# Performance work log

Hardware: AMD Instinct MI355X
Metric: run time of the kernel (lower is better)

Reference implementation:

```python
import jax, jax.numpy as jnp
import numpy as np

B, T, R, A = 4, 40, 2000, 36864
H = W = 64
C = 256
PP = 7
RED = 16.0
NCLS = 21
NPOS = 64   # rois_per_image*B//4
NNEG = 192  # rois_per_image*B*3//4
DH = 1024

def _iou(b1, b2):
    # boxes are (top,left,bottom,right)
    t = jnp.maximum(b1[..., 0], b2[..., 0])
    l = jnp.maximum(b1[..., 1], b2[..., 1])
    b = jnp.minimum(b1[..., 2], b2[..., 2])
    r = jnp.minimum(b1[..., 3], b2[..., 3])
    inter = jnp.clip(b - t, 0.0) * jnp.clip(r - l, 0.0)
    a1 = (b1[..., 2] - b1[..., 0]) * (b1[..., 3] - b1[..., 1])
    a2 = (b2[..., 2] - b2[..., 0]) * (b2[..., 3] - b2[..., 1])
    return inter / (a1 + a2 - inter)

def _smooth_l1(p, t):
    d = jnp.abs(p - t)
    return jnp.mean(jnp.where(d < 1.0, 0.5 * d * d, d - 0.5))

def _roi_pool(fm, rois):
    # fm [B,C,H,W], rois [N,5] = (img_id, top,left,bottom,right) in feature-map coords
    fmt = jnp.transpose(fm, (0, 2, 3, 1))  # [B,H,W,C]
    n = rois[:, 0].astype(jnp.int32)[:, None, None]
    t, l, b, r = rois[:, 1], rois[:, 2], rois[:, 3], rois[:, 4]
    g = (jnp.arange(PP, dtype=fm.dtype) + 0.5) / PP
    ys = jnp.clip(t[:, None] + g * (b - t)[:, None], 0.0, H - 1.0)
    xs = jnp.clip(l[:, None] + g * (r - l)[:, None], 0.0, W - 1.0)
    y0 = jnp.floor(ys).astype(jnp.int32)
    x0 = jnp.floor(xs).astype(jnp.int32)
    y1 = jnp.minimum(y0 + 1, H - 1)
    x1 = jnp.minimum(x0 + 1, W - 1)
    wy = (ys - y0)[:, :, None, None]
    wx = (xs - x0)[:, None, :, None]
    def gat(yi, xi):
        return fmt[n, yi[:, :, None], xi[:, None, :], :]  # [N,PP,PP,C]
    v = (gat(y0, x0) * (1 - wy) * (1 - wx) + gat(y0, x1) * (1 - wy) * wx
         + gat(y1, x0) * wy * (1 - wx) + gat(y1, x1) * wy * wx)
    return v.reshape(v.shape[0], -1)  # [N, PP*PP*C]

def _forward(nms_reg, nms_cls, feature_maps, bboxes, classes, anchors, rpn_reg, rpn_cls, W1, b1, Wr, br, Wc, bc):
    # ---------------- RPN trainer: anchor/target matching ----------------
    iou_a = _iou(bboxes[:, :, None, :], anchors[None, None, :, :])   # [B,T,A]
    max_iou = jnp.max(iou_a, axis=1)                                  # [B,A]
    tidx = jnp.argmax(iou_a, axis=1)
    max_tgt = jnp.take_along_axis(bboxes, jnp.broadcast_to(tidx[:, :, None], (B, A, 4)), axis=1)
    mask = (max_iou > 0.5).reshape(-1)
    pos = jnp.nonzero(mask, size=128)[0]        # first 128 positives, flat order (matches cls[mask][:128])
    neg = jnp.nonzero(~mask, size=256 - B)[0]   # torch quirk: 256 - len(mask_matched) = 256 - B
    clsf = rpn_cls.reshape(-1)
    logits = jnp.concatenate([clsf[pos], clsf[neg]])
    lbl = jnp.concatenate([jnp.ones(128, dtype=logits.dtype), jnp.zeros(256 - B, dtype=logits.dtype)])
    rpn_cls_loss = jnp.mean(jnp.maximum(logits, 0) - logits * lbl + jnp.log1p(jnp.exp(-jnp.abs(logits))))
    anc_f = jnp.broadcast_to(anchors[None], (B, A, 4)).reshape(-1, 4)
    rpn_reg_loss = _smooth_l1(rpn_reg.reshape(-1, 4)[pos], max_tgt.reshape(-1, 4)[pos] - anc_f[pos]) / 4.0

    # ------------- RCNN trainer: proposal matching + sampling -------------
    iou_r = _iou(nms_reg[:, None, :, :], bboxes[:, :, None, :])  # [B,T,R]
    iou_m = jnp.max(iou_r, axis=1)                               # [B,R]
    ridx = jnp.argmax(iou_r, axis=1)
    iou_f = iou_m.reshape(-1)
    posr = jnp.nonzero(iou_f > 0.5, size=NPOS)[0]                # first NPOS positives, flat order
    negscore = jnp.where(iou_f <= 0.5, iou_f, -jnp.inf)
    negr = jax.lax.top_k(negscore, NNEG)[1]                      # negatives sorted by IoU descending
    cls_g = jnp.take_along_axis(classes, ridx, axis=1).reshape(-1)
    cls_s = jnp.concatenate([cls_g[posr], jnp.zeros(NNEG, dtype=cls_g.dtype)])
    imid = jnp.repeat(jnp.arange(B, dtype=nms_reg.dtype), R)
    nmsf = nms_reg.reshape(-1, 4)
    sel = jnp.concatenate([posr, negr])
    rois = jnp.concatenate([imid[sel][:, None], nmsf[sel]], axis=1)  # [256,5]
    feat = _roi_pool(feature_maps, rois)
    hmid = jax.nn.relu(feat @ W1 + b1)
    rreg = hmid @ Wr + br
    rcls = hmid @ Wc + bc
    logp = jax.nn.log_softmax(rcls, axis=-1)
    rcnn_cls_loss = -jnp.mean(jnp.take_along_axis(logp, cls_s[:, None], axis=1))
    posb = nmsf[posr]
    rounded = jnp.concatenate([jnp.floor(posb[:, :2] * RED), jnp.ceil(posb[:, 2:] * RED)], axis=1) / RED
    mb = jnp.take_along_axis(bboxes, jnp.broadcast_to(ridx[:, :, None], (B, R, 4)), axis=1).reshape(-1, 4)[posr]
    tgt = mb - rounded
    pr = rreg[:NPOS]
    rcnn_reg_loss = sum(_smooth_l1(pr[:, c], tgt[:, c]) for c in range(4)) / 4.0
    offset = sum(jnp.mean(jnp.abs(pr[:, c] - tgt[:, c])) for c in range(4)) / 4.0
    acc = jnp.mean((jnp.argmax(rcls[:NPOS], axis=-1) == cls_s[:NPOS]).astype(jnp.float32))
    return rpn_cls_loss, rpn_reg_loss, rcnn_cls_loss, rcnn_reg_loss, acc, offset

def _boxes(k, shape):
    k1, k2 = jax.random.split(k)
    c = jax.random.uniform(k1, shape + (2,), minval=10.0, maxval=54.0)
    h = jax.random.uniform(k2, shape + (2,), minval=3.0, maxval=8.0)
    return jnp.concatenate([c - h, c + h], axis=-1)  # (top,left,bottom,right)

def setup_inputs():
    key = jax.random.key(0)
    ks = jax.random.split(key, 13)
    base = _boxes(ks[0], (T,))
    shift = jax.random.uniform(ks[1], (B, T, 2), minval=-0.2, maxval=0.2)
    bboxes = base[None] + jnp.concatenate([shift, shift], axis=-1)  # guarantees >=128 RPN positives
    classes = jax.random.randint(ks[2], (B, T), 1, NCLS)
    anchors = _boxes(ks[3], (A,)).at[:T].set(base)
    nms_reg = _boxes(ks[4], (B, R))
    shift2 = jax.random.uniform(ks[5], (B, T, 2), minval=-0.1, maxval=0.1)
    nms_reg = nms_reg.at[:, :T].set(bboxes + jnp.concatenate([shift2, shift2], axis=-1))  # >=64 RCNN positives
    nms_cls = jax.random.normal(ks[6], (B, R))
    feature_maps = jax.random.normal(ks[7], (B, C, H, W))
    rpn_reg = 0.1 * jax.random.normal(ks[8], (B, A, 4))
    rpn_cls = jax.random.normal(ks[9], (B, A))
    D = PP * PP * C
    W1 = jax.random.normal(ks[10], (D, DH)) * float(1.0 / np.sqrt(D))
    b1 = jnp.zeros((DH,))
    Wr = jax.random.normal(ks[11], (DH, 4)) * float(1.0 / np.sqrt(DH))
    br = jnp.zeros((4,))
    Wc = jax.random.normal(ks[12], (DH, NCLS)) * float(1.0 / np.sqrt(DH))
    bc = jnp.zeros((NCLS,))
    return dict(nms_reg=nms_reg, nms_cls=nms_cls, feature_maps=feature_maps, bboxes=bboxes,
                classes=classes, anchors=anchors, rpn_reg=rpn_reg, rpn_cls=rpn_cls,
                W1=W1, b1=b1, Wr=Wr, br=br, Wc=Wc, bc=bc)

def reference(nms_reg, nms_cls, feature_maps, bboxes, classes, anchors, rpn_reg, rpn_cls, W1, b1, Wr, br, Wc, bc):
    return _forward(nms_reg, nms_cls, feature_maps, bboxes, classes, anchors, rpn_reg, rpn_cls, W1, b1, Wr, br, Wc, bc)
```

## Files before the change

kernel.cpp:

```cpp
#include <hip/hip_runtime.h>

typedef unsigned short u16;
typedef unsigned long long u64;

constexpr int cB = 4, cT = 40, cR = 2000, cA = 36864;
constexpr int cH = 64, cW = 64, cC = 256, cPP = 7;
constexpr int cNCLS = 21, cNPOS = 64, cNNEG = 192, cDH = 1024;
constexpr int cD = cPP * cPP * cC;
constexpr int cBA = cB * cA;
constexpr int cBR = cB * cR;
constexpr int NW64 = cBA / 64;
constexpr int SPLITS = 8;
constexpr int KCH = cD / SPLITS;
constexpr int NCH = KCH / 32;
constexpr unsigned POSKEY = 0x007FFFFFu;

constexpr size_t O_TIDX  = 0;
constexpr size_t O_MASKW = (size_t)cBA * 4;
constexpr size_t O_FMT   = 0;
constexpr size_t O_CPART = 0;
constexpr size_t O_PERS  = 8388608;
constexpr size_t O_SEL   = O_PERS;
constexpr size_t O_CLS   = O_PERS + 1024;
constexpr size_t O_ROIS  = O_PERS + 2048;
constexpr size_t O_TGT   = O_PERS + 6144;
constexpr size_t O_FEAT  = O_PERS + 8192;
constexpr size_t O_RREG  = O_FEAT + (size_t)256 * cD * 2;
constexpr size_t O_RCLS  = O_RREG + 4096;
constexpr size_t O_KEYS  = O_RCLS + 24576;
constexpr size_t O_RIDXG = O_KEYS + 32000;

__device__ __forceinline__ float b2f(u16 u) {
  return __uint_as_float(((unsigned)u) << 16);
}
__device__ __forceinline__ u16 f2b(float f) {
  unsigned x = __float_as_uint(f);
  unsigned r = x + 0x7FFFu + ((x >> 16) & 1u);
  return (u16)(r >> 16);
}
__device__ __forceinline__ unsigned f2key(float f) {
  unsigned b = __float_as_uint(f);
  return b ^ ((b & 0x80000000u) ? 0xFFFFFFFFu : 0x80000000u);
}

typedef __attribute__((ext_vector_type(8))) short short8;
typedef __attribute__((ext_vector_type(4))) float f32x4;

__global__ void k_ious(const float* __restrict__ bboxes, const float* __restrict__ anchors,
                       const float* __restrict__ nms_reg,
                       int* __restrict__ tidx, u64* __restrict__ maskw,
                       unsigned* __restrict__ keys, int* __restrict__ ridxg) {
  __shared__ float sb[cB * cT * 4];
  if (blockIdx.x < 576) {
    int b = blockIdx.x / 144;
    if (threadIdx.x < cT * 4) sb[threadIdx.x] = bboxes[b * cT * 4 + threadIdx.x];
    __syncthreads();
    int i = blockIdx.x * 256 + threadIdx.x;
    int a = i - b * cA;
    float4 av = ((const float4*)anchors)[a];
    float at = av.x, al = av.y, ab = av.z, ar = av.w;
    float area_a = (ab - at) * (ar - al);
    float best = -1.0f; int bi = 0;
    for (int t = 0; t < cT; ++t) {
      float bt = sb[t * 4], bl = sb[t * 4 + 1], bbv = sb[t * 4 + 2], brv = sb[t * 4 + 3];
      float ih = fmaxf(fminf(bbv, ab) - fmaxf(bt, at), 0.0f);
      float iw = fmaxf(fminf(brv, ar) - fmaxf(bl, al), 0.0f);
      float inter = ih * iw;
      float a1 = (bbv - bt) * (brv - bl);
      float iou = inter / (a1 + area_a - inter);
      if (iou > best) { best = iou; bi = t; }
    }
    tidx[i] = bi;
    u64 bal = __ballot(best > 0.5f);
    if ((threadIdx.x & 63) == 0) maskw[i >> 6] = bal;
  } else {
    for (int j = threadIdx.x; j < cB * cT * 4; j += 256) sb[j] = bboxes[j];
    __syncthreads();
    int i = (blockIdx.x - 576) * 256 + threadIdx.x;
    if (i >= cBR) return;
    int b = i / cR;
    float4 nv = ((const float4*)nms_reg)[i];
    float nt = nv.x, nl = nv.y, nb = nv.z, nr = nv.w;
    float area_n = (nb - nt) * (nr - nl);
    float best = -1.0f; int bi = 0;
    for (int t = 0; t < cT; ++t) {
      const float* bx = &sb[(b * cT + t) * 4];
      float ih = fmaxf(fminf(bx[2], nb) - fmaxf(bx[0], nt), 0.0f);
      float iw = fmaxf(fminf(bx[3], nr) - fmaxf(bx[1], nl), 0.0f);
      float inter = ih * iw;
      float a1 = (bx[2] - bx[0]) * (bx[3] - bx[1]);
      float iou = inter / (a1 + area_n - inter);
      if (iou > best) { best = iou; bi = t; }
    }
    keys[i] = (best <= 0.5f) ? f2key(best) : POSKEY;
    ridxg[i] = bi;
  }
}

__global__ __launch_bounds__(1024) void k_select(
    const u64* __restrict__ maskw, const int* __restrict__ tidx,
    const float* __restrict__ rpn_cls, const float* __restrict__ rpn_reg,
    const float* __restrict__ bboxes, const float* __restrict__ anchors,
    const unsigned* __restrict__ keysg, const int* __restrict__ ridxg,
    const float* __restrict__ nms_reg, const int* __restrict__ classes,
    int* __restrict__ sel, int* __restrict__ cls_s,
    float* __restrict__ rois, float* __restrict__ tgt,
    float* __restrict__ out) {
  __shared__ __align__(16) char smem[50688];
  __shared__ float s_scalF[2];
  __shared__ int s_scalI[3];
  int tid = threadIdx.x, lane = tid & 63, w = tid >> 6;
  u64 lmask = (1ULL << lane) - 1ULL;

  if (blockIdx.x == 0) {
    u64* s_w   = (u64*)smem;
    int* s_pre = (int*)(smem + 18432);
    int* s_cw  = (int*)(smem + 19008);
    int* s_pos = (int*)(smem + 19584);
    int* s_neg = (int*)(smem + 20096);
    for (int k = tid; k < NW64; k += 1024) s_w[k] = maskw[k];
    if (tid < 128) s_pos[tid] = 0;
    if (tid < 252) s_neg[tid] = 0;
    if (tid == 0) { s_scalF[0] = 0.0f; s_scalF[1] = 0.0f; }
    __syncthreads();
    if (tid < 144) {
      int c = 0;
      #pragma unroll
      for (int k2 = 0; k2 < 16; ++k2) c += __popcll(s_w[tid * 16 + k2]);
      s_cw[tid] = c;
    }
    __syncthreads();
    if (tid == 0) {
      int run = 0;
      for (int ch = 0; ch < 144; ++ch) { s_pre[ch] = run; run += s_cw[ch]; }
    }
    __syncthreads();
    for (int ch = w; ch < 144; ch += 16) {
      int pbase = s_pre[ch];
      int nbase = ch * 1024 - pbase;
      if (pbase >= 128 && nbase >= 252) continue;
      int pc = 0;
      #pragma unroll
      for (int s2 = 0; s2 < 16; ++s2) {
        u64 word = s_w[ch * 16 + s2];
        bool m = (word >> lane) & 1ULL;
        int prefP = __popcll(word & lmask);
        int idx = ch * 1024 + s2 * 64 + lane;
        if (m) {
          int g = pbase + pc + prefP;
          if (g < 128) s_pos[g] = idx;
        } else {
          int g = nbase + (s2 * 64 + lane) - (pc + prefP);
          if (g < 252) s_neg[g] = idx;
        }
        pc += __popcll(word);
      }
    }
    __syncthreads();
    if (tid < 380) {
      int flat; float lbl;
      if (tid < 128) { flat = s_pos[tid]; lbl = 1.0f; }
      else           { flat = s_neg[tid - 128]; lbl = 0.0f; }
      float l = rpn_cls[flat];
      float term = fmaxf(l, 0.0f) - l * lbl + log1pf(expf(-fabsf(l)));
      atomicAdd(&s_scalF[0], term);
    }
    if (tid < 512) {
      int j = tid >> 2, c = tid & 3;
      int flat = s_pos[j];
      int b = flat / cA, a = flat - b * cA;
      int t = tidx[flat];
      float p = rpn_reg[flat * 4 + c];
      float tg = bboxes[(b * cT + t) * 4 + c] - anchors[a * 4 + c];
      float d = fabsf(p - tg);
      float sl = (d < 1.0f) ? 0.5f * d * d : d - 0.5f;
      atomicAdd(&s_scalF[1], sl);
    }
    __syncthreads();
    if (tid == 0) {
      out[0] = s_scalF[0] / 380.0f;
      out[1] = s_scalF[1] / 512.0f / 4.0f;
    }
  } else {
    unsigned* s_key = (unsigned*)smem;
    int* s_hist = (int*)(smem + 32000);
    int* s_pc   = (int*)(smem + 48384);
    int* s_wsum = (int*)(smem + 48896);
    int* s_wsuf = (int*)(smem + 48960);
    int* s_posr = (int*)(smem + 49024);
    int* s_negr = (int*)(smem + 49280);

    for (int i = tid; i < cBR; i += 1024) s_key[i] = keysg[i];
    if (tid < 64) s_posr[tid] = 0;
    __syncthreads();

    {
      int myv = 0; int mypre[8];
      #pragma unroll
      for (int p = 0; p < 8; ++p) {
        int i = p * 1024 + tid;
        bool v = (i < cBR) && (s_key[i] == POSKEY);
        u64 bal = __ballot(v);
        if (lane == 0) s_pc[p * 16 + w] = __popcll(bal);
        mypre[p] = __popcll(bal & lmask);
        myv |= v ? (1 << p) : 0;
      }
      __syncthreads();
      if (tid == 0) {
        int run = 0;
        for (int k = 0; k < 128; ++k) { int t = s_pc[k]; s_pc[k] = run; run += t; }
      }
      __syncthreads();
      #pragma unroll
      for (int p = 0; p < 8; ++p) {
        if (myv & (1 << p)) {
          int g = s_pc[p * 16 + w] + mypre[p];
          if (g < 64) s_posr[g] = p * 1024 + tid;
        }
      }
    }

    unsigned thr = 0; int G = 0;
    int need = cNNEG;
    #pragma unroll
    for (int lvl = 0; lvl < 3; ++lvl) {
      __syncthreads();
      #pragma unroll
      for (int k = 0; k < 4; ++k) s_hist[tid * 4 + k] = 0;
      __syncthreads();
      #pragma unroll
      for (int p = 0; p < 8; ++p) {
        int i = p * 1024 + tid;
        if (i < cBR) {
          unsigned key = s_key[i];
          int bkt = -1;
          if (lvl == 0) bkt = key >> 20;
          else if (lvl == 1) { if ((key >> 20) == (thr >> 20)) bkt = (key >> 8) & 0xFFF; }
          else { if ((key >> 8) == (thr >> 8)) bkt = (key & 0xFF) << 4; }
          if (bkt >= 0) atomicAdd(&s_hist[bkt], 1);
        }
      }
      __syncthreads();
      int local0 = s_hist[tid * 4 + 0], local1 = s_hist[tid * 4 + 1];
      int local2 = s_hist[tid * 4 + 2], local3 = s_hist[tid * 4 + 3];
      int lsum = local0 + local1 + local2 + local3;
      int x = lsum;
      #pragma unroll
      for (int off = 1; off < 64; off <<= 1) {
        int t = __shfl_down(x, off, 64);
        if (lane + off < 64) x += t;
      }
      if (lane == 0) s_wsum[w] = x;
      __syncthreads();
      if (tid == 0) {
        int run = 0;
        for (int wi = 15; wi >= 0; --wi) { s_wsuf[wi] = run; run += s_wsum[wi]; }
      }
      __syncthreads();
      int above = s_wsuf[w] + (x - lsum);
      int run = above;
      int loc[4] = {local3, local2, local1, local0};
      #pragma unroll
      for (int j = 0; j < 4; ++j) {
        int S = run + loc[j];
        if (run < need && S >= need) { s_scalI[0] = tid * 4 + (3 - j); s_scalI[1] = run; }
        run = S;
      }
      __syncthreads();
      int bS = s_scalI[0], ov = s_scalI[1];
      if (lvl == 0) thr = ((unsigned)bS) << 20;
      else if (lvl == 1) thr |= ((unsigned)bS) << 8;
      else thr |= ((unsigned)bS) >> 4;
      G += ov;
      need -= ov;
    }

    if (tid == 0) s_scalI[2] = 0;
    __syncthreads();
    #pragma unroll
    for (int p = 0; p < 8; ++p) {
      int i = p * 1024 + tid;
      if (i < cBR && s_key[i] > thr) {
        int slot = atomicAdd(&s_scalI[2], 1);
        s_negr[slot] = i;
      }
    }
    {
      __syncthreads();
      int myv = 0; int mypre[8];
      #pragma unroll
      for (int p = 0; p < 8; ++p) {
        int i = p * 1024 + tid;
        bool v = (i < cBR) && (s_key[i] == thr);
        u64 bal = __ballot(v);
        if (lane == 0) s_pc[p * 16 + w] = __popcll(bal);
        mypre[p] = __popcll(bal & lmask);
        myv |= v ? (1 << p) : 0;
      }
      __syncthreads();
      if (tid == 0) {
        int run = 0;
        for (int k = 0; k < 128; ++k) { int t = s_pc[k]; s_pc[k] = run; run += t; }
      }
      __syncthreads();
      #pragma unroll
      for (int p = 0; p < 8; ++p) {
        if (myv & (1 << p)) {
          int g = s_pc[p * 16 + w] + mypre[p];
          if (g < need) s_negr[G + g] = p * 1024 + tid;
        }
      }
    }
    __syncthreads();

    if (tid < 256) {
      int flat = (tid < 64) ? s_posr[tid] : s_negr[tid - 64];
      sel[tid] = flat;
      int b = flat / cR;
      #pragma unroll
      for (int c = 0; c < 4; ++c) rois[tid * 4 + c] = nms_reg[flat * 4 + c];
      cls_s[tid] = (tid < 64) ? classes[b * cT + ridxg[flat]] : 0;
      if (tid < 64) {
        int mt = ridxg[flat];
        #pragma unroll
        for (int c = 0; c < 4; ++c) {
          float v = nms_reg[flat * 4 + c];
          float rr = ((c < 2) ? floorf(v * 16.0f) : ceilf(v * 16.0f)) / 16.0f;
          float mbv = bboxes[(b * cT + mt) * 4 + c];
          tgt[tid * 4 + c] = mbv - rr;
        }
      }
    }
  }
}

__global__ __launch_bounds__(256) void k_fmt(const float* __restrict__ fm, u16* __restrict__ fmt) {
  __shared__ float tile[64][65];
  int b = blockIdx.z;
  int p0 = blockIdx.x * 64, c0 = blockIdx.y * 64;
  int t = threadIdx.x;
  int pL = (t & 15) * 4, cL = t >> 4;
  #pragma unroll
  for (int i = 0; i < 4; ++i) {
    int c = cL + i * 16;
    float4 v = *(const float4*)&fm[((size_t)b * cC + c0 + c) * (cH * cW) + p0 + pL];
    tile[c][pL] = v.x; tile[c][pL + 1] = v.y; tile[c][pL + 2] = v.z; tile[c][pL + 3] = v.w;
  }
  __syncthreads();
  int pW = t >> 2, cg = (t & 3) * 16;
  unsigned pk[8];
  #pragma unroll
  for (int j = 0; j < 8; ++j) {
    unsigned lo = f2b(tile[cg + 2 * j][pW]);
    unsigned hi = f2b(tile[cg + 2 * j + 1][pW]);
    pk[j] = lo | (hi << 16);
  }
  u16* dst = &fmt[((size_t)b * (cH * cW) + p0 + pW) * cC + c0 + cg];
  *(uint4*)dst = *(uint4*)&pk[0];
  *(uint4*)(dst + 8) = *(uint4*)&pk[4];
}

__global__ void k_roi_pool(const u16* __restrict__ fmt, const float* __restrict__ rois,
                           const int* __restrict__ sel, u16* __restrict__ feat) {
  int j = blockIdx.x;
  int py = blockIdx.y;
  int c = threadIdx.x;
  int flat = sel[j];
  int n = flat / cR;
  float t = rois[j * 4 + 0], l = rois[j * 4 + 1];
  float bb = rois[j * 4 + 2], r = rois[j * 4 + 3];
  const u16* base = fmt + (size_t)n * (cH * cW) * cC;
  float gy = (py + 0.5f) / (float)cPP;
  float ys = fminf(fmaxf(t + gy * (bb - t), 0.0f), 63.0f);
  int y0 = (int)floorf(ys);
  int y1 = min(y0 + 1, 63);
  float wy = ys - (float)y0;
  #pragma unroll
  for (int px = 0; px < cPP; ++px) {
    float gx = (px + 0.5f) / (float)cPP;
    float xs = fminf(fmaxf(l + gx * (r - l), 0.0f), 63.0f);
    int x0 = (int)floorf(xs);
    int x1 = min(x0 + 1, 63);
    float wx = xs - (float)x0;
    float f00 = b2f(base[(y0 * cW + x0) * cC + c]);
    float f01 = b2f(base[(y0 * cW + x1) * cC + c]);
    float f10 = b2f(base[(y1 * cW + x0) * cC + c]);
    float f11 = b2f(base[(y1 * cW + x1) * cC + c]);
    float v = f00 * (1.0f - wy) * (1.0f - wx) + f01 * (1.0f - wy) * wx +
              f10 * wy * (1.0f - wx) + f11 * wy * wx;
    feat[((size_t)j * 49 + py * cPP + px) * cC + c] = f2b(v);
  }
}

__global__ __launch_bounds__(256) void k_gemm1(const u16* __restrict__ feat, const float* __restrict__ W1,
                                               float* __restrict__ Cpart) {
  __shared__ u16 As[64][40];
  __shared__ u16 Bs[32][40];
  int tid = threadIdx.x;
  int n0 = blockIdx.x * 32;
  int kb0 = blockIdx.y * KCH;
  int m0 = blockIdx.z * 64;
  int lane = tid & 63, w = tid >> 6;
  int r = lane & 15, q = lane >> 4;
  f32x4 acc[2] = {};
  int arow = tid >> 2, ako = (tid & 3) * 8;
  int bn2 = tid & 31, bkq = tid >> 5;

  uint4 rA0, rA1;
  float rb0[4], rb1[4];
  auto loadAB = [&](int kc, uint4& ra, float* rb) {
    int kb = kb0 + kc * 32;
    ra = *(const uint4*)&feat[(size_t)(m0 + arow) * cD + kb + ako];
    const float* bp = &W1[(size_t)(kb + bkq * 4) * cDH + n0 + bn2];
    rb[0] = bp[0]; rb[1] = bp[cDH]; rb[2] = bp[2 * cDH]; rb[3] = bp[3 * cDH];
  };
  auto step = [&](int kc, uint4& ra, float* rb, bool pf) {
    __syncthreads();
    *(uint4*)&As[arow][ako] = ra;
    union { u16 u[4]; uint2 v; } pb;
    #pragma unroll
    for (int j = 0; j < 4; ++j) pb.u[j] = f2b(rb[j]);
    *(uint2*)&Bs[bn2][bkq * 4] = pb.v;
    if (pf) loadAB(kc + 2, ra, rb);
    __syncthreads();
    short8 a = *(const short8*)&As[w * 16 + r][q * 8];
    #pragma unroll
    for (int nt = 0; nt < 2; ++nt) {
      short8 bfr = *(const short8*)&Bs[nt * 16 + r][q * 8];
      acc[nt] = __builtin_amdgcn_mfma_f32_16x16x32_bf16(a, bfr, acc[nt], 0, 0, 0);
    }
  };

  loadAB(0, rA0, rb0);
  loadAB(1, rA1, rb1);
  for (int kc = 0; kc < NCH - 1; kc += 2) {
    step(kc, rA0, rb0, kc + 2 < NCH);
    step(kc + 1, rA1, rb1, kc + 3 < NCH);
  }
  step(NCH - 1, rA0, rb0, false);

  float* Cp = Cpart + (size_t)blockIdx.y * 256 * cDH;
  #pragma unroll
  for (int nt = 0; nt < 2; ++nt) {
    #pragma unroll
    for (int rg = 0; rg < 4; ++rg) {
      int row = m0 + w * 16 + q * 4 + rg;
      int col = n0 + nt * 16 + r;
      Cp[(size_t)row * cDH + col] = acc[nt][rg];
    }
  }
}

__global__ __launch_bounds__(256) void k_heads(
    const float* __restrict__ Cpart, const float* __restrict__ b1,
    const float* __restrict__ Wr, const float* __restrict__ br,
    const float* __restrict__ Wc, const float* __restrict__ bc,
    float* __restrict__ rreg, float* __restrict__ rcls) {
  __shared__ float sacc[25];
  int row = blockIdx.x, tid = threadIdx.x, lane = tid & 63;
  if (tid < 25) sacc[tid] = 0.0f;
  __syncthreads();
  int k0 = tid * 4;
  float4 h = *(const float4*)&b1[k0];
  #pragma unroll
  for (int s = 0; s < SPLITS; ++s) {
    float4 c = *(const float4*)&Cpart[(size_t)s * 256 * cDH + (size_t)row * cDH + k0];
    h.x += c.x; h.y += c.y; h.z += c.z; h.w += c.w;
  }
  float hv[4] = {fmaxf(h.x, 0.f), fmaxf(h.y, 0.f), fmaxf(h.z, 0.f), fmaxf(h.w, 0.f)};
  float part[25];
  #pragma unroll
  for (int c = 0; c < 25; ++c) part[c] = 0.0f;
  #pragma unroll
  for (int j = 0; j < 4; ++j) {
    float4 wr = *(const float4*)&Wr[(k0 + j) * 4];
    part[0] += hv[j] * wr.x; part[1] += hv[j] * wr.y;
    part[2] += hv[j] * wr.z; part[3] += hv[j] * wr.w;
    const float* wc = &Wc[(k0 + j) * 21];
    #pragma unroll
    for (int c = 0; c < 21; ++c) part[4 + c] += hv[j] * wc[c];
  }
  #pragma unroll
  for (int off = 32; off; off >>= 1) {
    #pragma unroll
    for (int c = 0; c < 25; ++c) part[c] += __shfl_down(part[c], off, 64);
  }
  if (lane == 0) {
    #pragma unroll
    for (int c = 0; c < 25; ++c) atomicAdd(&sacc[c], part[c]);
  }
  __syncthreads();
  if (tid < 4) rreg[row * 4 + tid] = sacc[tid] + br[tid];
  else if (tid < 25) rcls[row * 21 + (tid - 4)] = sacc[tid] + bc[tid - 4];
}

__global__ void k_final(const float* __restrict__ rcls, const float* __restrict__ rreg,
                        const int* __restrict__ cls_s, const float* __restrict__ tgt,
                        float* __restrict__ out) {
  __shared__ float s_cls, s_acc, s_sl1, s_off;
  int tid = threadIdx.x;
  if (tid == 0) { s_cls = 0.0f; s_acc = 0.0f; s_sl1 = 0.0f; s_off = 0.0f; }
  __syncthreads();
  {
    int row = tid;
    float m = -INFINITY;
    for (int c = 0; c < cNCLS; ++c) m = fmaxf(m, rcls[row * cNCLS + c]);
    float sum = 0.0f;
    for (int c = 0; c < cNCLS; ++c) sum += expf(rcls[row * cNCLS + c] - m);
    float lse = m + logf(sum);
    float closs = lse - rcls[row * cNCLS + cls_s[row]];
    atomicAdd(&s_cls, closs);
  }
  if (tid < 64) {
    int am = 0; float bv = rcls[tid * cNCLS];
    for (int c = 1; c < cNCLS; ++c) {
      float v = rcls[tid * cNCLS + c];
      if (v > bv) { bv = v; am = c; }
    }
    if (am == cls_s[tid]) atomicAdd(&s_acc, 1.0f);
    float sl = 0.0f, of = 0.0f;
    #pragma unroll
    for (int c = 0; c < 4; ++c) {
      float d = fabsf(rreg[tid * 4 + c] - tgt[tid * 4 + c]);
      sl += (d < 1.0f) ? 0.5f * d * d : d - 0.5f;
      of += d;
    }
    atomicAdd(&s_sl1, sl);
    atomicAdd(&s_off, of);
  }
  __syncthreads();
  if (tid == 0) {
    out[2] = s_cls / 256.0f;
    out[3] = s_sl1 / 256.0f;
    out[4] = s_acc / 64.0f;
    out[5] = s_off / 256.0f;
  }
}

extern "C" void kernel_launch(void* const* d_in, const int* in_sizes, int n_in,
                              void* d_out, int out_size, void* d_ws, size_t ws_size,
                              hipStream_t stream) {
  const float* nms_reg = (const float*)d_in[0];
  const float* fm      = (const float*)d_in[2];
  const float* bboxes  = (const float*)d_in[3];
  const int*   classes = (const int*)d_in[4];
  const float* anchors = (const float*)d_in[5];
  const float* rpn_reg = (const float*)d_in[6];
  const float* rpn_cls = (const float*)d_in[7];
  const float* W1      = (const float*)d_in[8];
  const float* b1      = (const float*)d_in[9];
  const float* Wr      = (const float*)d_in[10];
  const float* br      = (const float*)d_in[11];
  const float* Wc      = (const float*)d_in[12];
  const float* bc      = (const float*)d_in[13];
  float* out = (float*)d_out;
  char* ws = (char*)d_ws;

  int*      tidx  = (int*)(ws + O_TIDX);
  u64*      maskw = (u64*)(ws + O_MASKW);
  u16*      fmt   = (u16*)(ws + O_FMT);
  float*    Cpart = (float*)(ws + O_CPART);
  int*      sel   = (int*)(ws + O_SEL);
  int*      clss  = (int*)(ws + O_CLS);
  float*    rois  = (float*)(ws + O_ROIS);
  float*    tgt   = (float*)(ws + O_TGT);
  u16*      feat  = (u16*)(ws + O_FEAT);
  float*    rreg  = (float*)(ws + O_RREG);
  float*    rcls  = (float*)(ws + O_RCLS);
  unsigned* keys  = (unsigned*)(ws + O_KEYS);
  int*      ridxg = (int*)(ws + O_RIDXG);

  k_ious<<<576 + 32, 256, 0, stream>>>(bboxes, anchors, nms_reg, tidx, maskw, keys, ridxg);
  k_select<<<2, 1024, 0, stream>>>(maskw, tidx, rpn_cls, rpn_reg, bboxes, anchors,
                                   keys, ridxg, nms_reg, classes, sel, clss, rois, tgt, out);
  k_fmt<<<dim3(cH * cW / 64, cC / 64, cB), 256, 0, stream>>>(fm, fmt);
  k_roi_pool<<<dim3(256, cPP), 256, 0, stream>>>(fmt, rois, sel, feat);
  k_gemm1<<<dim3(32, SPLITS, 4), 256, 0, stream>>>(feat, W1, Cpart);
  k_heads<<<256, 256, 0, stream>>>(Cpart, b1, Wr, br, Wc, bc, rreg, rcls);
  k_final<<<1, 256, 0, stream>>>(rcls, rreg, clss, tgt, out);
}
```

Measured before the change: 201.3 us.

## Fuse fmt transpose into IoU kernel, fold final loss into heads, retile GEMM

Merges the feature-map transpose/bf16 conversion into the IoU kernel as extra blocks, and folds the loss reduction into the heads kernel, which now accumulates into the output with atomics. Output zeroing moves to k_select. Launch count drops as a result. The split-K GEMM now uses 128-wide K tiles with XOR-swizzled LDS, register prefetch and 14 splits, to cut synchronisation per MFMA and raise parallelism. The workspace is relaid so the transposed map no longer aliases earlier buffers. Float atomics make the loss sums order-dependent.

```diff
diff --git a/kernel.cpp b/kernel.cpp
--- a/kernel.cpp
+++ b/kernel.cpp
@@ -10,25 +10,23 @@
 constexpr int cBA = cB * cA;
 constexpr int cBR = cB * cR;
 constexpr int NW64 = cBA / 64;
-constexpr int SPLITS = 8;
+constexpr int SPLITS = 14;
 constexpr int KCH = cD / SPLITS;
-constexpr int NCH = KCH / 32;
+constexpr int BK = 128;
+constexpr int NITER = KCH / BK;
 constexpr unsigned POSKEY = 0x007FFFFFu;
 
 constexpr size_t O_TIDX  = 0;
-constexpr size_t O_MASKW = (size_t)cBA * 4;
-constexpr size_t O_FMT   = 0;
-constexpr size_t O_CPART = 0;
-constexpr size_t O_PERS  = 8388608;
-constexpr size_t O_SEL   = O_PERS;
-constexpr size_t O_CLS   = O_PERS + 1024;
-constexpr size_t O_ROIS  = O_PERS + 2048;
-constexpr size_t O_TGT   = O_PERS + 6144;
-constexpr size_t O_FEAT  = O_PERS + 8192;
-constexpr size_t O_RREG  = O_FEAT + (size_t)256 * cD * 2;
-constexpr size_t O_RCLS  = O_RREG + 4096;
-constexpr size_t O_KEYS  = O_RCLS + 24576;
-constexpr size_t O_RIDXG = O_KEYS + 32000;
+constexpr size_t O_MASKW = 589824;
+constexpr size_t O_KEYS  = 608256;
+constexpr size_t O_RIDXG = 640256;
+constexpr size_t O_SEL   = 672256;
+constexpr size_t O_CLS   = 673280;
+constexpr size_t O_ROIS  = 674304;
+constexpr size_t O_TGT   = 678400;
+constexpr size_t O_FMT   = 1048576;
+constexpr size_t O_FEAT  = O_FMT + 8388608;
+constexpr size_t O_CPART = O_FEAT + 6422528;
 
 __device__ __forceinline__ float b2f(u16 u) {
   return __uint_as_float(((unsigned)u) << 16);
@@ -46,16 +44,20 @@
 typedef __attribute__((ext_vector_type(8))) short short8;
 typedef __attribute__((ext_vector_type(4))) float f32x4;
 
-__global__ void k_ious(const float* __restrict__ bboxes, const float* __restrict__ anchors,
-                       const float* __restrict__ nms_reg,
-                       int* __restrict__ tidx, u64* __restrict__ maskw,
-                       unsigned* __restrict__ keys, int* __restrict__ ridxg) {
-  __shared__ float sb[cB * cT * 4];
-  if (blockIdx.x < 576) {
-    int b = blockIdx.x / 144;
+__global__ __launch_bounds__(256) void k_front(
+    const float* __restrict__ bboxes, const float* __restrict__ anchors,
+    const float* __restrict__ nms_reg, const float* __restrict__ fm,
+    int* __restrict__ tidx, u64* __restrict__ maskw,
+    unsigned* __restrict__ keys, int* __restrict__ ridxg,
+    u16* __restrict__ fmt) {
+  __shared__ float sfm[64 * 65];
+  int bid = blockIdx.x;
+  if (bid < 576) {
+    float* sb = sfm;
+    int b = bid / 144;
     if (threadIdx.x < cT * 4) sb[threadIdx.x] = bboxes[b * cT * 4 + threadIdx.x];
     __syncthreads();
-    int i = blockIdx.x * 256 + threadIdx.x;
+    int i = bid * 256 + threadIdx.x;
     int a = i - b * cA;
     float4 av = ((const float4*)anchors)[a];
     float at = av.x, al = av.y, ab = av.z, ar = av.w;
@@ -73,10 +75,11 @@
     tidx[i] = bi;
     u64 bal = __ballot(best > 0.5f);
     if ((threadIdx.x & 63) == 0) maskw[i >> 6] = bal;
-  } else {
+  } else if (bid < 608) {
+    float* sb = sfm;
     for (int j = threadIdx.x; j < cB * cT * 4; j += 256) sb[j] = bboxes[j];
     __syncthreads();
-    int i = (blockIdx.x - 576) * 256 + threadIdx.x;
+    int i = (bid - 576) * 256 + threadIdx.x;
     if (i >= cBR) return;
     int b = i / cR;
     float4 nv = ((const float4*)nms_reg)[i];
@@ -94,6 +97,32 @@
     }
     keys[i] = (best <= 0.5f) ? f2key(best) : POSKEY;
     ridxg[i] = bi;
+  } else {
+    int f = bid - 608;
+    int b = f >> 8;
+    int c0 = ((f >> 6) & 3) * 64;
+    int p0 = (f & 63) * 64;
+    int t = threadIdx.x;
+    int pL = (t & 15) * 4, cL = t >> 4;
+    #pragma unroll
+    for (int i = 0; i < 4; ++i) {
+      int c = cL + i * 16;
+      float4 v = *(const float4*)&fm[((size_t)b * cC + c0 + c) * (cH * cW) + p0 + pL];
+      sfm[c * 65 + pL] = v.x; sfm[c * 65 + pL + 1] = v.y;
+      sfm[c * 65 + pL + 2] = v.z; sfm[c * 65 + pL + 3] = v.w;
+    }
+    __syncthreads();
+    int pW = t >> 2, cg = (t & 3) * 16;
+    unsigned pk[8];
+    #pragma unroll
+    for (int j = 0; j < 8; ++j) {
+      unsigned lo = f2b(sfm[(cg + 2 * j) * 65 + pW]);
+      unsigned hi = f2b(sfm[(cg + 2 * j + 1) * 65 + pW]);
+      pk[j] = lo | (hi << 16);
+    }
+    u16* dst = &fmt[((size_t)b * (cH * cW) + p0 + pW) * cC + c0 + cg];
+    *(uint4*)dst = *(uint4*)&pk[0];
+    *(uint4*)(dst + 8) = *(uint4*)&pk[4];
   }
 }
 
@@ -113,6 +142,7 @@
   u64 lmask = (1ULL << lane) - 1ULL;
 
   if (blockIdx.x == 0) {
+    if (tid < 4) out[2 + tid] = 0.0f;
     u64* s_w   = (u64*)smem;
     int* s_pre = (int*)(smem + 18432);
     int* s_cw  = (int*)(smem + 19008);
@@ -332,32 +362,6 @@
       }
     }
   }
-}
-
-__global__ __launch_bounds__(256) void k_fmt(const float* __restrict__ fm, u16* __restrict__ fmt) {
-  __shared__ float tile[64][65];
-  int b = blockIdx.z;
-  int p0 = blockIdx.x * 64, c0 = blockIdx.y * 64;
-  int t = threadIdx.x;
-  int pL = (t & 15) * 4, cL = t >> 4;
-  #pragma unroll
-  for (int i = 0; i < 4; ++i) {
-    int c = cL + i * 16;
-    float4 v = *(const float4*)&fm[((size_t)b * cC + c0 + c) * (cH * cW) + p0 + pL];
-    tile[c][pL] = v.x; tile[c][pL + 1] = v.y; tile[c][pL + 2] = v.z; tile[c][pL + 3] = v.w;
-  }
-  __syncthreads();
-  int pW = t >> 2, cg = (t & 3) * 16;
-  unsigned pk[8];
-  #pragma unroll
-  for (int j = 0; j < 8; ++j) {
-    unsigned lo = f2b(tile[cg + 2 * j][pW]);
-    unsigned hi = f2b(tile[cg + 2 * j + 1][pW]);
-    pk[j] = lo | (hi << 16);
-  }
-  u16* dst = &fmt[((size_t)b * (cH * cW) + p0 + pW) * cC + c0 + cg];
-  *(uint4*)dst = *(uint4*)&pk[0];
-  *(uint4*)(dst + 8) = *(uint4*)&pk[4];
 }
 
 __global__ void k_roi_pool(const u16* __restrict__ fmt, const float* __restrict__ rois,
@@ -394,8 +398,8 @@
 
 __global__ __launch_bounds__(256) void k_gemm1(const u16* __restrict__ feat, const float* __restrict__ W1,
                                                float* __restrict__ Cpart) {
-  __shared__ u16 As[64][40];
-  __shared__ u16 Bs[32][40];
+  __shared__ u16 As[64 * 128];
+  __shared__ u16 Bs[32 * 128];
   int tid = threadIdx.x;
   int n0 = blockIdx.x * 32;
   int kb0 = blockIdx.y * KCH;
@@ -403,41 +407,53 @@
   int lane = tid & 63, w = tid >> 6;
   int r = lane & 15, q = lane >> 4;
   f32x4 acc[2] = {};
-  int arow = tid >> 2, ako = (tid & 3) * 8;
-  int bn2 = tid & 31, bkq = tid >> 5;
-
-  uint4 rA0, rA1;
-  float rb0[4], rb1[4];
-  auto loadAB = [&](int kc, uint4& ra, float* rb) {
-    int kb = kb0 + kc * 32;
-    ra = *(const uint4*)&feat[(size_t)(m0 + arow) * cD + kb + ako];
-    const float* bp = &W1[(size_t)(kb + bkq * 4) * cDH + n0 + bn2];
-    rb[0] = bp[0]; rb[1] = bp[cDH]; rb[2] = bp[2 * cDH]; rb[3] = bp[3 * cDH];
+
+  int am = tid >> 2;
+  int aj0 = (tid & 3) * 4;
+  int bn = tid & 31;
+  int bkg = tid >> 5;
+
+  uint4 ra[4];
+  float rb[16];
+  auto loadAB = [&](int it) {
+    int kb = kb0 + it * BK;
+    const u16* ap = &feat[(size_t)(m0 + am) * cD + kb];
+    #pragma unroll
+    for (int i = 0; i < 4; ++i) ra[i] = *(const uint4*)(ap + (aj0 + i) * 8);
+    const float* bp = &W1[(size_t)(kb + bkg * 16) * cDH + n0 + bn];
+    #pragma unroll
+    for (int j = 0; j < 16; ++j) rb[j] = bp[(size_t)j * cDH];
   };
-  auto step = [&](int kc, uint4& ra, float* rb, bool pf) {
-    __syncthreads();
-    *(uint4*)&As[arow][ako] = ra;
-    union { u16 u[4]; uint2 v; } pb;
-    #pragma unroll
-    for (int j = 0; j < 4; ++j) pb.u[j] = f2b(rb[j]);
-    *(uint2*)&Bs[bn2][bkq * 4] = pb.v;
-    if (pf) loadAB(kc + 2, ra, rb);
-    __syncthreads();
-    short8 a = *(const short8*)&As[w * 16 + r][q * 8];
-    #pragma unroll
-    for (int nt = 0; nt < 2; ++nt) {
-      short8 bfr = *(const short8*)&Bs[nt * 16 + r][q * 8];
-      acc[nt] = __builtin_amdgcn_mfma_f32_16x16x32_bf16(a, bfr, acc[nt], 0, 0, 0);
-    }
-  };
-
-  loadAB(0, rA0, rb0);
-  loadAB(1, rA1, rb1);
-  for (int kc = 0; kc < NCH - 1; kc += 2) {
-    step(kc, rA0, rb0, kc + 2 < NCH);
-    step(kc + 1, rA1, rb1, kc + 3 < NCH);
-  }
-  step(NCH - 1, rA0, rb0, false);
+
+  loadAB(0);
+  for (int it = 0; it < NITER; ++it) {
+    __syncthreads();
+    #pragma unroll
+    for (int i = 0; i < 4; ++i) {
+      int c = aj0 + i;
+      *(uint4*)&As[am * 128 + ((c ^ (am & 15)) << 3)] = ra[i];
+    }
+    #pragma unroll
+    for (int s = 0; s < 2; ++s) {
+      union { u16 u[8]; uint4 v; } pb;
+      #pragma unroll
+      for (int j = 0; j < 8; ++j) pb.u[j] = f2b(rb[s * 8 + j]);
+      int c = bkg * 2 + s;
+      *(uint4*)&Bs[bn * 128 + ((c ^ (bn & 15)) << 3)] = pb.v;
+    }
+    __syncthreads();
+    if (it + 1 < NITER) loadAB(it + 1);
+    #pragma unroll
+    for (int ks = 0; ks < 4; ++ks) {
+      int ca = ks * 4 + q;
+      short8 a = *(const short8*)&As[(w * 16 + r) * 128 + ((ca ^ r) << 3)];
+      #pragma unroll
+      for (int nt = 0; nt < 2; ++nt) {
+        short8 bfr = *(const short8*)&Bs[(nt * 16 + r) * 128 + ((ca ^ r) << 3)];
+        acc[nt] = __builtin_amdgcn_mfma_f32_16x16x32_bf16(a, bfr, acc[nt], 0, 0, 0);
+      }
+    }
+  }
 
   float* Cp = Cpart + (size_t)blockIdx.y * 256 * cDH;
   #pragma unroll
@@ -455,7 +471,8 @@
     const float* __restrict__ Cpart, const float* __restrict__ b1,
     const float* __restrict__ Wr, const float* __restrict__ br,
     const float* __restrict__ Wc, const float* __restrict__ bc,
-    float* __restrict__ rreg, float* __restrict__ rcls) {
+    const int* __restrict__ cls_s, const float* __restrict__ tgt,
+    float* __restrict__ out) {
   __shared__ float sacc[25];
   int row = blockIdx.x, tid = threadIdx.x, lane = tid & 63;
   if (tid < 25) sacc[tid] = 0.0f;
@@ -490,50 +507,34 @@
     for (int c = 0; c < 25; ++c) atomicAdd(&sacc[c], part[c]);
   }
   __syncthreads();
-  if (tid < 4) rreg[row * 4 + tid] = sacc[tid] + br[tid];
-  else if (tid < 25) rcls[row * 21 + (tid - 4)] = sacc[tid] + bc[tid - 4];
-}
-
-__global__ void k_final(const float* __restrict__ rcls, const float* __restrict__ rreg,
-                        const int* __restrict__ cls_s, const float* __restrict__ tgt,
-                        float* __restrict__ out) {
-  __shared__ float s_cls, s_acc, s_sl1, s_off;
-  int tid = threadIdx.x;
-  if (tid == 0) { s_cls = 0.0f; s_acc = 0.0f; s_sl1 = 0.0f; s_off = 0.0f; }
-  __syncthreads();
-  {
-    int row = tid;
+  if (tid == 0) {
+    int cls = cls_s[row];
     float m = -INFINITY;
-    for (int c = 0; c < cNCLS; ++c) m = fmaxf(m, rcls[row * cNCLS + c]);
+    float vals[21];
+    #pragma unroll
+    for (int c = 0; c < 21; ++c) { vals[c] = sacc[4 + c] + bc[c]; m = fmaxf(m, vals[c]); }
     float sum = 0.0f;
-    for (int c = 0; c < cNCLS; ++c) sum += expf(rcls[row * cNCLS + c] - m);
+    #pragma unroll
+    for (int c = 0; c < 21; ++c) sum += expf(vals[c] - m);
     float lse = m + logf(sum);
-    float closs = lse - rcls[row * cNCLS + cls_s[row]];
-    atomicAdd(&s_cls, closs);
-  }
-  if (tid < 64) {
-    int am = 0; float bv = rcls[tid * cNCLS];
-    for (int c = 1; c < cNCLS; ++c) {
-      float v = rcls[tid * cNCLS + c];
-      if (v > bv) { bv = v; am = c; }
-    }
-    if (am == cls_s[tid]) atomicAdd(&s_acc, 1.0f);
+    atomicAdd(&out[2], (lse - vals[cls]) * (1.0f / 256.0f));
+    if (row < 64) {
+      int am2 = 0; float bv = vals[0];
+      #pragma unroll
+      for (int c = 1; c < 21; ++c) if (vals[c] > bv) { bv = vals[c]; am2 = c; }
+      if (am2 == cls) atomicAdd(&out[4], 1.0f / 64.0f);
+    }
+  }
+  if (tid == 1 && row < 64) {
     float sl = 0.0f, of = 0.0f;
     #pragma unroll
     for (int c = 0; c < 4; ++c) {
-      float d = fabsf(rreg[tid * 4 + c] - tgt[tid * 4 + c]);
+      float d = fabsf((sacc[c] + br[c]) - tgt[row * 4 + c]);
       sl += (d < 1.0f) ? 0.5f * d * d : d - 0.5f;
       of += d;
     }
-    atomicAdd(&s_sl1, sl);
-    atomicAdd(&s_off, of);
-  }
-  __syncthreads();
-  if (tid == 0) {
-    out[2] = s_cls / 256.0f;
-    out[3] = s_sl1 / 256.0f;
-    out[4] = s_acc / 64.0f;
-    out[5] = s_off / 256.0f;
+    atomicAdd(&out[3], sl * (1.0f / 256.0f));
+    atomicAdd(&out[5], of * (1.0f / 256.0f));
   }
 }
 
@@ -558,24 +559,21 @@
 
   int*      tidx  = (int*)(ws + O_TIDX);
   u64*      maskw = (u64*)(ws + O_MASKW);
-  u16*      fmt   = (u16*)(ws + O_FMT);
-  float*    Cpart = (float*)(ws + O_CPART);
+  unsigned* keys  = (unsigned*)(ws + O_KEYS);
+  int*      ridxg = (int*)(ws + O_RIDXG);
   int*      sel   = (int*)(ws + O_SEL);
   int*      clss  = (int*)(ws + O_CLS);
   float*    rois  = (float*)(ws + O_ROIS);
   float*    tgt   = (float*)(ws + O_TGT);
+  u16*      fmt   = (u16*)(ws + O_FMT);
   u16*      feat  = (u16*)(ws + O_FEAT);
-  float*    rreg  = (float*)(ws + O_RREG);
-  float*    rcls  = (float*)(ws + O_RCLS);
-  unsigned* keys  = (unsigned*)(ws + O_KEYS);
-  int*      ridxg = (int*)(ws + O_RIDXG);
-
-  k_ious<<<576 + 32, 256, 0, stream>>>(bboxes, anchors, nms_reg, tidx, maskw, keys, ridxg);
+  float*    Cpart = (float*)(ws + O_CPART);
+
+  k_front<<<608 + 1024, 256, 0, stream>>>(bboxes, anchors, nms_reg, fm,
+                                          tidx, maskw, keys, ridxg, fmt);
   k_select<<<2, 1024, 0, stream>>>(maskw, tidx, rpn_cls, rpn_reg, bboxes, anchors,
                                    keys, ridxg, nms_reg, classes, sel, clss, rois, tgt, out);
-  k_fmt<<<dim3(cH * cW / 64, cC / 64, cB), 256, 0, stream>>>(fm, fmt);
   k_roi_pool<<<dim3(256, cPP), 256, 0, stream>>>(fmt, rois, sel, feat);
   k_gemm1<<<dim3(32, SPLITS, 4), 256, 0, stream>>>(feat, W1, Cpart);
-  k_heads<<<256, 256, 0, stream>>>(Cpart, b1, Wr, br, Wc, bc, rreg, rcls);
-  k_final<<<1, 256, 0, stream>>>(rcls, rreg, clss, tgt, out);
-}
+  k_heads<<<256, 256, 0, stream>>>(Cpart, b1, Wr, br, Wc, bc, clss, tgt, out);
+}
```

New measurement: 247.5 us. 22.9% more time.
